# Performance work log

Measured on AMD Instinct MI355X. Metric: run time of the kernel, lower is better.

The kernel has to match this reference:

```python
import jax, jax.numpy as jnp
import numpy as np

INPUT_SIZE = 512
HIDDEN_SIZE = 2048
OUTPUT_SIZE = 512
NUM_LAYERS = 4
INNER = INPUT_SIZE + HIDDEN_SIZE  # 2560
BATCH = 4096


def setup_inputs() -> dict:
    key = jax.random.key(0)
    ks = jax.random.split(key, 5)
    scale = 1.0 / np.sqrt(INNER)  # kaiming-uniform-like scale for nn.Linear
    x = jax.random.normal(ks[0], (BATCH, INPUT_SIZE), dtype=jnp.float32)
    h = jax.random.normal(ks[1], (BATCH, HIDDEN_SIZE), dtype=jnp.float32)
    W_layers = jax.random.normal(ks[2], (NUM_LAYERS, INNER, INNER), dtype=jnp.float32) * scale
    b_layers = jnp.zeros((NUM_LAYERS, INNER), dtype=jnp.float32)
    W_i2h = jax.random.normal(ks[3], (HIDDEN_SIZE, INNER), dtype=jnp.float32) * scale
    b_i2h = jnp.zeros((HIDDEN_SIZE,), dtype=jnp.float32)
    W_i2o = jax.random.normal(ks[4], (OUTPUT_SIZE, INNER), dtype=jnp.float32) * scale
    b_i2o = jnp.zeros((OUTPUT_SIZE,), dtype=jnp.float32)
    return {"x": x, "h": h, "W_layers": W_layers, "b_layers": b_layers,
            "W_i2h": W_i2h, "b_i2h": b_i2h, "W_i2o": W_i2o, "b_i2o": b_i2o}


def reference(x, h, W_layers, b_layers, W_i2h, b_i2h, W_i2o, b_i2o):
    # combined: [B, inner]
    combined = jnp.concatenate([x, h], axis=1)
    # stack of square Hebbian linear layers + ReLU (imprint trace writes are
    # state side effects only; they do not affect the forward output)
    for l in range(W_layers.shape[0]):
        combined = jax.nn.relu(jnp.einsum('bi,oi->bo', combined, W_layers[l]) + b_layers[l])
    hidden = jnp.tanh(jnp.einsum('bi,oi->bo', combined, W_i2h) + b_i2h)
    output = jnp.einsum('bi,oi->bo', combined, W_i2o) + b_i2o
    return (output, hidden)
```

## Files before the change

### kernel.cpp

```cpp
#include <hip/hip_runtime.h>
#include <hip/hip_bf16.h>

#define BATCH 4096
#define IN_SZ 512
#define HID_SZ 2048
#define OUT_SZ 512
#define NLAYER 4
#define INNER 2560
#define NKT (INNER / 64)


typedef __attribute__((ext_vector_type(8))) short bf16x8;
typedef __attribute__((ext_vector_type(4))) float f32x4;

__device__ __forceinline__ unsigned short f2bf(float f) {
  unsigned int u = __float_as_uint(f);
  u += 0x7fff + ((u >> 16) & 1);
  return (unsigned short)(u >> 16);
}

__device__ __forceinline__ void gload16(const void* g, void* l) {
  __builtin_amdgcn_global_load_lds(
      (const __attribute__((address_space(1))) unsigned int*)g,
      (__attribute__((address_space(3))) unsigned int*)l,
      16, 0, 0);
}


__global__ void cvt_f32_bf16(const float* __restrict__ in,
                             unsigned short* __restrict__ out, int n4) {
  int i = blockIdx.x * blockDim.x + threadIdx.x;
  const int stride = gridDim.x * blockDim.x;
  for (; i < n4; i += stride) {
    float4 v = *reinterpret_cast<const float4*>(in + (long)i * 4);
    ushort4 o;
    o.x = f2bf(v.x); o.y = f2bf(v.y); o.z = f2bf(v.z); o.w = f2bf(v.w);
    *reinterpret_cast<ushort4*>(out + (long)i * 4) = o;
  }
}

__global__ void build_combined(const float* __restrict__ x,
                               const float* __restrict__ h,
                               unsigned short* __restrict__ out) {
  const int n4 = BATCH * INNER / 4;
  int i = blockIdx.x * blockDim.x + threadIdx.x;
  const int stride = gridDim.x * blockDim.x;
  for (; i < n4; i += stride) {
    int row = i / (INNER / 4);
    int c4 = i - row * (INNER / 4);
    const float* src = (c4 < IN_SZ / 4) ? (x + (long)row * IN_SZ + c4 * 4)
                                        : (h + (long)row * HID_SZ + (c4 - IN_SZ / 4) * 4);
    float4 v = *reinterpret_cast<const float4*>(src);
    ushort4 o;
    o.x = f2bf(v.x); o.y = f2bf(v.y); o.z = f2bf(v.z); o.w = f2bf(v.w);
    *reinterpret_cast<ushort4*>(out + (long)i * 4) = o;
  }
}


#define STAGE_U(kt, u, buf) do {                                              \
  if ((u) < 4) {                                                              \
    const int base_ = (u) * 32 + w * 8;                                       \
    gload16(A + (long)(row0 + base_ + srow) * INNER + (kt) * 64 + srcsw,      \
            (void*)(&lds[buf][base_ * 64]));                                  \
  } else {                                                                    \
    const int base_ = ((u) - 4) * 32 + w * 8;                                 \
    gload16(B + (long)(col0 + base_ + srow) * INNER + (kt) * 64 + srcsw,      \
            (void*)(&lds[buf][8192 + base_ * 64]));                           \
  } } while (0)

#define LOAD_AF(dst, mh, buf) do {                                           \
  const unsigned short* Ar_ = &lds[buf][0];                                  \
  _Pragma("unroll")                                                          \
  for (int m_ = 0; m_ < 2; ++m_) {                                           \
    int r_ = wr * 64 + (mh) * 32 + m_ * 16 + fr;                             \
    dst[m_][0] = *(const bf16x8*)(Ar_ + r_ * 64 + csw0);                     \
    dst[m_][1] = *(const bf16x8*)(Ar_ + r_ * 64 + csw1);                     \
  } } while (0)

#define LOAD_BQA(dst, buf) do {                                              \
  const unsigned short* Br_ = &lds[buf][8192];                               \
  _Pragma("unroll")                                                          \
  for (int n_ = 0; n_ < 3; ++n_) {                                           \
    int r_ = wcn * 80 + n_ * 16 + fr;                                        \
    dst[n_][0] = *(const bf16x8*)(Br_ + r_ * 64 + csw0);                     \
    dst[n_][1] = *(const bf16x8*)(Br_ + r_ * 64 + csw1);                     \
  } } while (0)

#define LOAD_BQB(dst, buf) do {                                              \
  const unsigned short* Br_ = &lds[buf][8192];                               \
  _Pragma("unroll")                                                          \
  for (int n_ = 0; n_ < 2; ++n_) {                                           \
    int r_ = wcn * 80 + (3 + n_) * 16 + fr;                                  \
    dst[n_][0] = *(const bf16x8*)(Br_ + r_ * 64 + csw0);                     \
    dst[n_][1] = *(const bf16x8*)(Br_ + r_ * 64 + csw1);                     \
  } } while (0)

#define MF_A(af, bq, mh) do {                                                 \
  __builtin_amdgcn_s_setprio(1);                                              \
  _Pragma("unroll")                                                           \
  for (int m_ = 0; m_ < 2; ++m_)                                              \
    _Pragma("unroll")                                                         \
    for (int n_ = 0; n_ < 3; ++n_) {                                          \
      acc[(mh) * 2 + m_][n_] = __builtin_amdgcn_mfma_f32_16x16x32_bf16(       \
          af[m_][0], bq[n_][0], acc[(mh) * 2 + m_][n_], 0, 0, 0);             \
      acc[(mh) * 2 + m_][n_] = __builtin_amdgcn_mfma_f32_16x16x32_bf16(       \
          af[m_][1], bq[n_][1], acc[(mh) * 2 + m_][n_], 0, 0, 0);             \
    }                                                                         \
  __builtin_amdgcn_s_setprio(0);                                              \
} while (0)

#define MF_B(af, bq, mh) do {                                                 \
  __builtin_amdgcn_s_setprio(1);                                              \
  _Pragma("unroll")                                                           \
  for (int m_ = 0; m_ < 2; ++m_)                                              \
    _Pragma("unroll")                                                         \
    for (int n_ = 0; n_ < 2; ++n_) {                                          \
      acc[(mh) * 2 + m_][3 + n_] = __builtin_amdgcn_mfma_f32_16x16x32_bf16(   \
          af[m_][0], bq[n_][0], acc[(mh) * 2 + m_][3 + n_], 0, 0, 0);         \
      acc[(mh) * 2 + m_][3 + n_] = __builtin_amdgcn_mfma_f32_16x16x32_bf16(   \
          af[m_][1], bq[n_][1], acc[(mh) * 2 + m_][3 + n_], 0, 0, 0);         \
    }                                                                         \
  __builtin_amdgcn_s_setprio(0);                                              \
} while (0)

#define SB() __builtin_amdgcn_sched_barrier(0)

#define TILE_BODY(d, AC, QC, AN, QN) do {                                     \
  const int T = T2 + (d);                                                     \
  const int kt1 = (T + 1 < NKT) ? T + 1 : NKT - 1;                            \
  const int kt2 = (T + 2 < NKT) ? T + 2 : NKT - 1;                            \
         \
  LOAD_BQB(bqB, d);                                                           \
  STAGE_U(kt1, 6, (d) ^ 1); STAGE_U(kt1, 7, (d) ^ 1); STAGE_U(kt1, 8, (d) ^ 1); \
  SB();                                                                       \
  __builtin_amdgcn_s_barrier();                                               \
  asm volatile("s_waitcnt lgkmcnt(4)" ::: "memory");          \
  SB();                                                                       \
  MF_A(AC, QC, 0);                                                            \
  __builtin_amdgcn_s_barrier();                                               \
           \
  LOAD_AF(afB, 1, d);                                                         \
  STAGE_U(kt1, 0, (d) ^ 1); STAGE_U(kt1, 1, (d) ^ 1);                         \
  SB();                                                                       \
  __builtin_amdgcn_s_barrier();                                               \
  asm volatile("s_waitcnt lgkmcnt(4)" ::: "memory");            \
  SB();                                                                       \
  MF_B(AC, bqB, 0);                                                           \
  __builtin_amdgcn_s_barrier();                                               \
                          \
  STAGE_U(kt2, 4, d); STAGE_U(kt2, 5, d);                                     \
  SB();                                                                       \
  __builtin_amdgcn_s_barrier();                                               \
  asm volatile("s_waitcnt lgkmcnt(0)" ::: "memory");            \
  SB();                                                                       \
  MF_B(afB, bqB, 1);                                                          \
  __builtin_amdgcn_s_barrier();                                               \
    \
  STAGE_U(kt2, 2, d); STAGE_U(kt2, 3, d);                                     \
  asm volatile("s_waitcnt vmcnt(4)" ::: "memory");      \
  __builtin_amdgcn_s_barrier();                                               \
  SB();                                                                       \
  LOAD_AF(AN, 0, (d) ^ 1);                                                    \
  LOAD_BQA(QN, (d) ^ 1);                                                      \
  SB();                           \
  MF_A(afB, QC, 1);                                                           \
  __builtin_amdgcn_s_barrier();                                               \
} while (0)

template <int MODE>
__global__ __launch_bounds__(256, 2)
void gemm8(const unsigned short* __restrict__ A, const unsigned short* __restrict__ B,
           const float* __restrict__ bias0, const float* __restrict__ bias1,
           void* __restrict__ C) {
  __shared__ unsigned short lds[2][18432];

  const int tid = threadIdx.x;
  const int w = tid >> 6;
  const int lane = tid & 63;

  const int flat = blockIdx.x;
  const int xcd = flat & 7;
  const int local = flat >> 3;
  const int nb = xcd * 2 + (local & 1);
  const int mb = local >> 1;
  const int row0 = mb * 128, col0 = nb * 160;
  const int wr = w >> 1, wcn = w & 1;

  const int srow = lane >> 3;
  const int srcsw = ((((lane & 7) << 4) ^ ((lane >> 3) << 4)) >> 1);

  const int fr = lane & 15;
  const int csw0 = ((((lane >> 4) << 4)) ^ ((lane & 7) << 4)) >> 1;
  const int csw1 = ((64 + ((lane >> 4) << 4)) ^ ((lane & 7) << 4)) >> 1;

  f32x4 acc[4][5] = {};
  bf16x8 afA0[2][2], afA1[2][2], afB[2][2];
  bf16x8 bqA0[3][2], bqA1[3][2], bqB[2][2];

  STAGE_U(0, 0, 0); STAGE_U(0, 1, 0); STAGE_U(0, 2, 0); STAGE_U(0, 3, 0);
  STAGE_U(0, 4, 0); STAGE_U(0, 5, 0); STAGE_U(0, 6, 0); STAGE_U(0, 7, 0);
  STAGE_U(0, 8, 0);
  STAGE_U(1, 4, 1); STAGE_U(1, 5, 1); STAGE_U(1, 2, 1); STAGE_U(1, 3, 1);
  asm volatile("s_waitcnt vmcnt(4)" ::: "memory");
  __builtin_amdgcn_s_barrier();
  SB();
  LOAD_AF(afA0, 0, 0);
  LOAD_BQA(bqA0, 0);
  SB();

  for (int T2 = 0; T2 < NKT; T2 += 2) {
    TILE_BODY(0, afA0, bqA0, afA1, bqA1);
    TILE_BODY(1, afA1, bqA1, afA0, bqA0);
  }
  asm volatile("s_waitcnt vmcnt(0)" ::: "memory");

  const int erow = row0 + wr * 64 + ((lane >> 4) << 2);
  const int ecol = col0 + wcn * 80 + fr;
  if (MODE == 0) {
    unsigned short* Co = (unsigned short*)C;
#pragma unroll
    for (int n = 0; n < 5; ++n) {
      const int col = ecol + n * 16;
      const float bv = bias0[col];
#pragma unroll
      for (int m = 0; m < 4; ++m) {
        const int row = erow + m * 16;
#pragma unroll
        for (int j = 0; j < 4; ++j) {
          float v = acc[m][n][j] + bv;
          v = fmaxf(v, 0.0f);
          Co[(long)(row + j) * INNER + col] = f2bf(v);
        }
      }
    }
  } else {
    float* outO = (float*)C;
    float* outH = (float*)C + (long)BATCH * OUT_SZ;
#pragma unroll
    for (int n = 0; n < 5; ++n) {
      const int col = ecol + n * 16;
      if (col < OUT_SZ) {
        const float bv = bias0[col];
#pragma unroll
        for (int m = 0; m < 4; ++m) {
          const int row = erow + m * 16;
#pragma unroll
          for (int j = 0; j < 4; ++j)
            outO[(long)(row + j) * OUT_SZ + col] = acc[m][n][j] + bv;
        }
      } else {
        const int hc = col - OUT_SZ;
        const float bv = bias1[hc];
#pragma unroll
        for (int m = 0; m < 4; ++m) {
          const int row = erow + m * 16;
#pragma unroll
          for (int j = 0; j < 4; ++j)
            outH[(long)(row + j) * HID_SZ + hc] = tanhf(acc[m][n][j] + bv);
        }
      }
    }
  }
}


extern "C" void kernel_launch(void* const* d_in, const int* in_sizes, int n_in,
                              void* d_out, int out_size, void* d_ws, size_t ws_size,
                              hipStream_t stream) {
  const float* x   = (const float*)d_in[0];
  const float* h   = (const float*)d_in[1];
  const float* Wl  = (const float*)d_in[2];
  const float* bl  = (const float*)d_in[3];
  const float* Wih = (const float*)d_in[4];
  const float* bih = (const float*)d_in[5];
  const float* Wio = (const float*)d_in[6];
  const float* bio = (const float*)d_in[7];

  unsigned short* ws   = (unsigned short*)d_ws;
  unsigned short* Wlb  = ws;
  unsigned short* Whb  = Wlb + (long)NLAYER * INNER * INNER;
  unsigned short* act0 = Whb + (long)INNER * INNER;
  unsigned short* act1 = act0 + (long)BATCH * INNER;

  cvt_f32_bf16<<<2048, 256, 0, stream>>>(Wl,  Wlb, NLAYER * INNER * INNER / 4);
  cvt_f32_bf16<<<256,  256, 0, stream>>>(Wio, Whb, OUT_SZ * INNER / 4);
  cvt_f32_bf16<<<1024, 256, 0, stream>>>(Wih, Whb + (long)OUT_SZ * INNER, HID_SZ * INNER / 4);
  build_combined<<<2048, 256, 0, stream>>>(x, h, act0);

  unsigned short* a_in = act0;
  unsigned short* a_out = act1;
  for (int l = 0; l < NLAYER; ++l) {
    gemm8<0><<<512, 256, 0, stream>>>(a_in, Wlb + (long)l * INNER * INNER,
                                      bl + (long)l * INNER, nullptr, a_out);
    unsigned short* t = a_in; a_in = a_out; a_out = t;
  }

  gemm8<1><<<512, 256, 0, stream>>>(a_in, Whb, bio, bih, d_out);
}
```

Baseline: 305.9 us.

## Load B operand fragments directly from global memory into registers, bypassing LDS

The GEMM kernel stops staging the weight (B) tile through LDS. Each wave now loads its B MFMA fragments straight from global memory into double-buffered registers, while only the activation (A) tile goes through LDS. This cuts LDS traffic and the number of barriers per k-tile and simplifies the pipeline. In exchange it issues uncoalesced 16-byte global loads spread across rows, adds register pressure, and leaves a full vmcnt(0) wait plus a barrier on every tile. The three weight-conversion launches are also merged into one kernel.

```diff
diff --git a/kernel.cpp b/kernel.cpp
--- a/kernel.cpp
+++ b/kernel.cpp
@@ -27,15 +27,24 @@
 }
 
 
-__global__ void cvt_f32_bf16(const float* __restrict__ in,
-                             unsigned short* __restrict__ out, int n4) {
+#define NWL4  6553600
+#define NWO4  327680
+#define NWH4  1310720
+__global__ void cvt_all(const float* __restrict__ Wl, const float* __restrict__ Wih,
+                        const float* __restrict__ Wio, unsigned short* __restrict__ dst) {
+  const int n4 = NWL4 + NWO4 + NWH4;
   int i = blockIdx.x * blockDim.x + threadIdx.x;
   const int stride = gridDim.x * blockDim.x;
   for (; i < n4; i += stride) {
-    float4 v = *reinterpret_cast<const float4*>(in + (long)i * 4);
+    const float* src;
+    long off4;
+    if (i < NWL4) { src = Wl; off4 = i; }
+    else if (i < NWL4 + NWO4) { src = Wio; off4 = i - NWL4; }
+    else { src = Wih; off4 = i - NWL4 - NWO4; }
+    float4 v = *reinterpret_cast<const float4*>(src + off4 * 4);
     ushort4 o;
     o.x = f2bf(v.x); o.y = f2bf(v.y); o.z = f2bf(v.z); o.w = f2bf(v.w);
-    *reinterpret_cast<ushort4*>(out + (long)i * 4) = o;
+    *reinterpret_cast<ushort4*>(dst + (long)i * 4) = o;
   }
 }
 
@@ -58,15 +67,12 @@
 }
 
 
-#define STAGE_U(kt, u, buf) do {                                              \
-  if ((u) < 4) {                                                              \
-    const int base_ = (u) * 32 + w * 8;                                       \
+#define STAGE_A4(kt, buf) do {                                                \
+  _Pragma("unroll")                                                           \
+  for (int u_ = 0; u_ < 4; ++u_) {                                            \
+    const int base_ = u_ * 32 + w * 8;                                        \
     gload16(A + (long)(row0 + base_ + srow) * INNER + (kt) * 64 + srcsw,      \
             (void*)(&lds[buf][base_ * 64]));                                  \
-  } else {                                                                    \
-    const int base_ = ((u) - 4) * 32 + w * 8;                                 \
-    gload16(B + (long)(col0 + base_ + srow) * INNER + (kt) * 64 + srcsw,      \
-            (void*)(&lds[buf][8192 + base_ * 64]));                           \
   } } while (0)
 
 #define LOAD_AF(dst, mh, buf) do {                                           \
@@ -78,30 +84,19 @@
     dst[m_][1] = *(const bf16x8*)(Ar_ + r_ * 64 + csw1);                     \
   } } while (0)
 
-#define LOAD_BQA(dst, buf) do {                                              \
-  const unsigned short* Br_ = &lds[buf][8192];                               \
+#define LOAD_BG(dst, kt) do {                                                \
   _Pragma("unroll")                                                          \
-  for (int n_ = 0; n_ < 3; ++n_) {                                           \
-    int r_ = wcn * 80 + n_ * 16 + fr;                                        \
-    dst[n_][0] = *(const bf16x8*)(Br_ + r_ * 64 + csw0);                     \
-    dst[n_][1] = *(const bf16x8*)(Br_ + r_ * 64 + csw1);                     \
+  for (int n_ = 0; n_ < 5; ++n_) {                                           \
+    dst[n_][0] = *(const bf16x8*)(Bbase + (long)n_ * 16 * INNER + (kt) * 64);      \
+    dst[n_][1] = *(const bf16x8*)(Bbase + (long)n_ * 16 * INNER + (kt) * 64 + 32); \
   } } while (0)
 
-#define LOAD_BQB(dst, buf) do {                                              \
-  const unsigned short* Br_ = &lds[buf][8192];                               \
-  _Pragma("unroll")                                                          \
-  for (int n_ = 0; n_ < 2; ++n_) {                                           \
-    int r_ = wcn * 80 + (3 + n_) * 16 + fr;                                  \
-    dst[n_][0] = *(const bf16x8*)(Br_ + r_ * 64 + csw0);                     \
-    dst[n_][1] = *(const bf16x8*)(Br_ + r_ * 64 + csw1);                     \
-  } } while (0)
-
-#define MF_A(af, bq, mh) do {                                                 \
+#define MF_HALF(af, bq, mh) do {                                              \
   __builtin_amdgcn_s_setprio(1);                                              \
   _Pragma("unroll")                                                           \
   for (int m_ = 0; m_ < 2; ++m_)                                              \
     _Pragma("unroll")                                                         \
-    for (int n_ = 0; n_ < 3; ++n_) {                                          \
+    for (int n_ = 0; n_ < 5; ++n_) {                                          \
       acc[(mh) * 2 + m_][n_] = __builtin_amdgcn_mfma_f32_16x16x32_bf16(       \
           af[m_][0], bq[n_][0], acc[(mh) * 2 + m_][n_], 0, 0, 0);             \
       acc[(mh) * 2 + m_][n_] = __builtin_amdgcn_mfma_f32_16x16x32_bf16(       \
@@ -110,70 +105,34 @@
   __builtin_amdgcn_s_setprio(0);                                              \
 } while (0)
 
-#define MF_B(af, bq, mh) do {                                                 \
-  __builtin_amdgcn_s_setprio(1);                                              \
-  _Pragma("unroll")                                                           \
-  for (int m_ = 0; m_ < 2; ++m_)                                              \
-    _Pragma("unroll")                                                         \
-    for (int n_ = 0; n_ < 2; ++n_) {                                          \
-      acc[(mh) * 2 + m_][3 + n_] = __builtin_amdgcn_mfma_f32_16x16x32_bf16(   \
-          af[m_][0], bq[n_][0], acc[(mh) * 2 + m_][3 + n_], 0, 0, 0);         \
-      acc[(mh) * 2 + m_][3 + n_] = __builtin_amdgcn_mfma_f32_16x16x32_bf16(   \
-          af[m_][1], bq[n_][1], acc[(mh) * 2 + m_][3 + n_], 0, 0, 0);         \
-    }                                                                         \
-  __builtin_amdgcn_s_setprio(0);                                              \
-} while (0)
-
 #define SB() __builtin_amdgcn_sched_barrier(0)
 
-#define TILE_BODY(d, AC, QC, AN, QN) do {                                     \
+#define TILE_BODY(d, BC, BN) do {                                             \
   const int T = T2 + (d);                                                     \
-  const int kt1 = (T + 1 < NKT) ? T + 1 : NKT - 1;                            \
-  const int kt2 = (T + 2 < NKT) ? T + 2 : NKT - 1;                            \
-         \
-  LOAD_BQB(bqB, d);                                                           \
-  STAGE_U(kt1, 6, (d) ^ 1); STAGE_U(kt1, 7, (d) ^ 1); STAGE_U(kt1, 8, (d) ^ 1); \
+  const int kt1 = (T + 1 < NKT) ? T + 1 : NKT - 1;  \
+      \
+  STAGE_A4(kt1, (d) ^ 1);                                                     \
+  LOAD_BG(BN, kt1);                                                           \
+                                   \
+  LOAD_AF(afL, 0, d);                                                         \
+  LOAD_AF(afH, 1, d);                                                         \
   SB();                                                                       \
-  __builtin_amdgcn_s_barrier();                                               \
-  asm volatile("s_waitcnt lgkmcnt(4)" ::: "memory");          \
+  asm volatile("s_waitcnt lgkmcnt(4)" ::: "memory");           \
   SB();                                                                       \
-  MF_A(AC, QC, 0);                                                            \
-  __builtin_amdgcn_s_barrier();                                               \
-           \
-  LOAD_AF(afB, 1, d);                                                         \
-  STAGE_U(kt1, 0, (d) ^ 1); STAGE_U(kt1, 1, (d) ^ 1);                         \
+  MF_HALF(afL, BC, 0);                                                        \
+  asm volatile("s_waitcnt lgkmcnt(0)" ::: "memory");           \
   SB();                                                                       \
-  __builtin_amdgcn_s_barrier();                                               \
-  asm volatile("s_waitcnt lgkmcnt(4)" ::: "memory");            \
-  SB();                                                                       \
-  MF_B(AC, bqB, 0);                                                           \
-  __builtin_amdgcn_s_barrier();                                               \
-                          \
-  STAGE_U(kt2, 4, d); STAGE_U(kt2, 5, d);                                     \
-  SB();                                                                       \
-  __builtin_amdgcn_s_barrier();                                               \
-  asm volatile("s_waitcnt lgkmcnt(0)" ::: "memory");            \
-  SB();                                                                       \
-  MF_B(afB, bqB, 1);                                                          \
-  __builtin_amdgcn_s_barrier();                                               \
-    \
-  STAGE_U(kt2, 2, d); STAGE_U(kt2, 3, d);                                     \
-  asm volatile("s_waitcnt vmcnt(4)" ::: "memory");      \
-  __builtin_amdgcn_s_barrier();                                               \
-  SB();                                                                       \
-  LOAD_AF(AN, 0, (d) ^ 1);                                                    \
-  LOAD_BQA(QN, (d) ^ 1);                                                      \
-  SB();                           \
-  MF_A(afB, QC, 1);                                                           \
+  MF_HALF(afH, BC, 1);                                                        \
+  asm volatile("s_waitcnt vmcnt(0)" ::: "memory");        \
   __builtin_amdgcn_s_barrier();                                               \
 } while (0)
 
 template <int MODE>
 __global__ __launch_bounds__(256, 2)
-void gemm8(const unsigned short* __restrict__ A, const unsigned short* __restrict__ B,
-           const float* __restrict__ bias0, const float* __restrict__ bias1,
-           void* __restrict__ C) {
-  __shared__ unsigned short lds[2][18432];
+void gemm_bg(const unsigned short* __restrict__ A, const unsigned short* __restrict__ B,
+             const float* __restrict__ bias0, const float* __restrict__ bias1,
+             void* __restrict__ C) {
+  __shared__ unsigned short lds[2][8192];
 
   const int tid = threadIdx.x;
   const int w = tid >> 6;
@@ -194,26 +153,23 @@
   const int csw0 = ((((lane >> 4) << 4)) ^ ((lane & 7) << 4)) >> 1;
   const int csw1 = ((64 + ((lane >> 4) << 4)) ^ ((lane & 7) << 4)) >> 1;
 
+  const unsigned short* Bbase =
+      B + (long)(col0 + wcn * 80 + fr) * INNER + ((lane >> 4) * 8);
+
   f32x4 acc[4][5] = {};
-  bf16x8 afA0[2][2], afA1[2][2], afB[2][2];
-  bf16x8 bqA0[3][2], bqA1[3][2], bqB[2][2];
-
-  STAGE_U(0, 0, 0); STAGE_U(0, 1, 0); STAGE_U(0, 2, 0); STAGE_U(0, 3, 0);
-  STAGE_U(0, 4, 0); STAGE_U(0, 5, 0); STAGE_U(0, 6, 0); STAGE_U(0, 7, 0);
-  STAGE_U(0, 8, 0);
-  STAGE_U(1, 4, 1); STAGE_U(1, 5, 1); STAGE_U(1, 2, 1); STAGE_U(1, 3, 1);
-  asm volatile("s_waitcnt vmcnt(4)" ::: "memory");
+  bf16x8 afL[2][2], afH[2][2];
+  bf16x8 bq0[5][2], bq1[5][2];
+
+  STAGE_A4(0, 0);
+  LOAD_BG(bq0, 0);
+  asm volatile("s_waitcnt vmcnt(0)" ::: "memory");
   __builtin_amdgcn_s_barrier();
   SB();
-  LOAD_AF(afA0, 0, 0);
-  LOAD_BQA(bqA0, 0);
-  SB();
 
   for (int T2 = 0; T2 < NKT; T2 += 2) {
-    TILE_BODY(0, afA0, bqA0, afA1, bqA1);
-    TILE_BODY(1, afA1, bqA1, afA0, bqA0);
-  }
-  asm volatile("s_waitcnt vmcnt(0)" ::: "memory");
+    TILE_BODY(0, bq0, bq1);
+    TILE_BODY(1, bq1, bq0);
+  }
 
   const int erow = row0 + wr * 64 + ((lane >> 4) << 2);
   const int ecol = col0 + wcn * 80 + fr;
@@ -283,18 +239,16 @@
   unsigned short* act0 = Whb + (long)INNER * INNER;
   unsigned short* act1 = act0 + (long)BATCH * INNER;
 
-  cvt_f32_bf16<<<2048, 256, 0, stream>>>(Wl,  Wlb, NLAYER * INNER * INNER / 4);
-  cvt_f32_bf16<<<256,  256, 0, stream>>>(Wio, Whb, OUT_SZ * INNER / 4);
-  cvt_f32_bf16<<<1024, 256, 0, stream>>>(Wih, Whb + (long)OUT_SZ * INNER, HID_SZ * INNER / 4);
+  cvt_all<<<2048, 256, 0, stream>>>(Wl, Wih, Wio, Wlb);
   build_combined<<<2048, 256, 0, stream>>>(x, h, act0);
 
   unsigned short* a_in = act0;
   unsigned short* a_out = act1;
   for (int l = 0; l < NLAYER; ++l) {
-    gemm8<0><<<512, 256, 0, stream>>>(a_in, Wlb + (long)l * INNER * INNER,
-                                      bl + (long)l * INNER, nullptr, a_out);
+    gemm_bg<0><<<512, 256, 0, stream>>>(a_in, Wlb + (long)l * INNER * INNER,
+                                        bl + (long)l * INNER, nullptr, a_out);
     unsigned short* t = a_in; a_in = a_out; a_out = t;
   }
 
-  gemm8<1><<<512, 256, 0, stream>>>(a_in, Whb, bio, bih, d_out);
-}
+  gemm_bg<1><<<512, 256, 0, stream>>>(a_in, Whb, bio, bih, d_out);
+}
```

New measurement: 634.5 us. 2.07x slower.
